# Performance work log

Hardware: AMD Instinct MI355X
Metric: run time of the kernel (lower is better)

Reference implementation:

```python
import jax, jax.numpy as jnp
import numpy as np

WIN = 11
SIGMA = 1.5
K1, K2 = 0.01, 0.03
DATA_RANGE = 1.0


def _gauss1d(size, sigma):
    coords = jnp.arange(size, dtype=jnp.float32) - size // 2
    g = jnp.exp(-(coords ** 2) / (2.0 * sigma ** 2))
    return g / g.sum()


def _blur(x, g):
    # Separable depthwise Gaussian blur, VALID padding, matching F.conv2d(groups=C).
    C = x.shape[1]
    w = g.astype(x.dtype)
    kh = jnp.broadcast_to(w.reshape(1, 1, WIN, 1), (C, 1, WIN, 1))  # blur along H
    kw = jnp.broadcast_to(w.reshape(1, 1, 1, WIN), (C, 1, 1, WIN))  # blur along W
    dn = ('NCHW', 'OIHW', 'NCHW')
    out = jax.lax.conv_general_dilated(x, kh, (1, 1), 'VALID',
                                       dimension_numbers=dn, feature_group_count=C)
    out = jax.lax.conv_general_dilated(out, kw, (1, 1), 'VALID',
                                       dimension_numbers=dn, feature_group_count=C)
    return out


def setup_inputs() -> dict:
    key = jax.random.key(0)
    k1, k2 = jax.random.split(key)
    shape = (16, 3, 512, 512)
    image1 = jax.random.uniform(k1, shape, dtype=jnp.float32)
    image2 = jax.random.uniform(k2, shape, dtype=jnp.float32)
    window = _gauss1d(WIN, SIGMA)
    return {"image1": image1, "image2": image2, "window": window}


def reference(image1, image2, window):
    c1 = (K1 * DATA_RANGE) ** 2
    c2 = (K2 * DATA_RANGE) ** 2
    mu1 = _blur(image1, window)
    mu2 = _blur(image2, window)
    mu1_sq = mu1 * mu1
    mu2_sq = mu2 * mu2
    mu1_mu2 = mu1 * mu2
    sigma1_sq = _blur(image1 * image1, window) - mu1_sq
    sigma2_sq = _blur(image2 * image2, window) - mu2_sq
    sigma12 = _blur(image1 * image2, window) - mu1_mu2
    cs_map = (2.0 * sigma12 + c2) / (sigma1_sq + sigma2_sq + c2)
    ssim_map = (2.0 * mu1_mu2 + c1) / (mu1_sq + mu2_sq + c1) * cs_map
    # flatten(2).mean(-1) then .mean() over (B,C) == full mean (uniform sizes)
    return ssim_map.mean()
```

## Files before the change

kernel.cpp:

```cpp
#include <hip/hip_runtime.h>

#define WIN   11
#define IW    512
#define IH    512
#define OW    502
#define OH    502
#define NCH   48
#define TW    54
#define SWC   64
#define SWP   66
#define CH    8
#define NCHUNK 8
#define SLABH (CH*NCHUNK)
#define NGX   10
#define NGY   8
#define PXL   7

typedef float v2f __attribute__((ext_vector_type(2)));

__device__ __forceinline__ float fast_rcp(float x) {
    return __builtin_amdgcn_rcpf(x);
}

template<bool EDGE>
__device__ __forceinline__ void ssim_slab(const float* __restrict__ p1,
                                          const float* __restrict__ p2,
                                          const float (&w)[WIN],
                                          v2f (*vbuf)[CH][SWP],
                                          int x0, int y0, int tid, float& acc)
{
    const int c = tid;
    int gx = x0 + c;
    if (EDGE) gx = min(gx, IW - 1);

    v2f h[10];
#pragma unroll
    for (int j = 0; j < 10; ++j) {
        int gy = y0 + j; if (EDGE) gy = min(gy, IH - 1);
        const int gidx = gy * IW + gx;
        h[j].x = p1[gidx];
        h[j].y = p2[gidx];
    }

    const int rh = tid >> 3;
    const int gg = tid & 7;
    const int xs = gg * PXL;
    const float c1 = 0.0001f;
    const float c2 = 0.0009f;

#pragma unroll
    for (int ci = 0; ci < NCHUNK; ++ci) {
        const int jbase = y0 + 10 + ci * CH;
        v2f n[CH];
#pragma unroll
        for (int j = 0; j < CH; ++j) {
            int gy = jbase + j; if (EDGE) gy = min(gy, IH - 1);
            const int gidx = gy * IW + gx;
            n[j].x = p1[gidx];
            n[j].y = p2[gidx];
        }

        v2f accA[CH], accB[CH];
#pragma unroll
        for (int r = 0; r < CH; ++r) {
            accA[r] = (v2f){0.f, 0.f};
            accB[r] = (v2f){0.f, 0.f};
        }
#pragma unroll
        for (int j = 0; j < CH + 10; ++j) {
            v2f ab = (j < 10) ? h[j] : n[j - 10];
            v2f st;
            st.x = fmaf(ab.x, ab.x, ab.y * ab.y);
            st.y = ab.x * ab.y;
#pragma unroll
            for (int k = 0; k < WIN; ++k) {
                const int r = j - k;
                if (r >= 0 && r < CH) {
                    v2f ws; ws.x = w[k]; ws.y = w[k];
                    accA[r] = __builtin_elementwise_fma(ws, ab, accA[r]);
                    accB[r] = __builtin_elementwise_fma(ws, st, accB[r]);
                }
            }
            if (j >= 10) {
                vbuf[0][j - 10][c] = accA[j - 10];
                vbuf[1][j - 10][c] = accB[j - 10];
            }
        }
#pragma unroll
        for (int j = 0; j < 10; ++j)
            h[j] = (j < 2) ? h[8 + j] : n[j - 2];

        __syncthreads();

        {
            v2f resA[PXL], resB[PXL];
#pragma unroll
            for (int q = 0; q < 2; ++q) {
                v2f x2[PXL + 10];
                const v2f* src = &vbuf[q][rh][xs];
#pragma unroll
                for (int t = 0; t < PXL + 10; ++t)
                    x2[t] = src[t];
#pragma unroll
                for (int o = 0; o < PXL; ++o) {
                    v2f s = {0.f, 0.f};
#pragma unroll
                    for (int k = 0; k < WIN; ++k) {
                        v2f ws; ws.x = w[k]; ws.y = w[k];
                        s = __builtin_elementwise_fma(ws, x2[o + k], s);
                    }
                    if (q == 0) resA[o] = s; else resB[o] = s;
                }
            }

            const int oy = y0 + ci * CH + rh;
#pragma unroll
            for (int o = 0; o < PXL; ++o) {
                const int tc = xs + o;
                bool valid = (tc < TW);
                if (EDGE) valid = valid && (oy < OH) && ((x0 + tc) < OW);
                if (valid) {
                    float m1 = resA[o].x, m2 = resA[o].y;
                    float mu11 = m1 * m1, mu22 = m2 * m2, mu12 = m1 * m2;
                    float sAB = resB[o].x - mu11 - mu22;
                    float s12 = resB[o].y - mu12;
                    float num = (2.f * mu12 + c1) * (2.f * s12 + c2);
                    float den = (mu11 + mu22 + c1) * (sAB + c2);
                    acc += num * fast_rcp(den);
                }
            }
        }
        __syncthreads();
    }
}

__global__ __launch_bounds__(64, 4)
void ssim_fused_kernel(const float* __restrict__ img1,
                       const float* __restrict__ img2,
                       const float* __restrict__ win,
                       float* __restrict__ partial)
{
    __shared__ __align__(16) v2f vbuf[2][CH][SWP];
    const int tid = threadIdx.x;
    const int ch = blockIdx.z;
    const int x0 = blockIdx.x * TW;
    const int y0 = blockIdx.y * SLABH;
    const float* __restrict__ p1 = img1 + (size_t)ch * (IW * IH);
    const float* __restrict__ p2 = img2 + (size_t)ch * (IW * IH);

    float w[WIN];
#pragma unroll
    for (int k = 0; k < WIN; ++k) w[k] = win[k];

    float acc = 0.f;
    const bool edge = (blockIdx.x == gridDim.x - 1) || (blockIdx.y == gridDim.y - 1);
    if (edge) ssim_slab<true >(p1, p2, w, vbuf, x0, y0, tid, acc);
    else      ssim_slab<false>(p1, p2, w, vbuf, x0, y0, tid, acc);

#pragma unroll
    for (int off = 32; off > 0; off >>= 1)
        acc += __shfl_down(acc, off, 64);
    if (tid == 0) {
        partial[(size_t)blockIdx.z * (gridDim.x * gridDim.y)
                + blockIdx.y * gridDim.x + blockIdx.x] = acc;
    }
}

__global__ __launch_bounds__(256)
void reduce_partials_kernel(const float* __restrict__ partial, int n4,
                            float* __restrict__ out, double inv_count)
{
    __shared__ double sd[256];
    const float4* p4 = reinterpret_cast<const float4*>(partial);
    double s = 0.0;
    for (int i = threadIdx.x; i < n4; i += 256) {
        float4 f = p4[i];
        s += (double)f.x + (double)f.y + (double)f.z + (double)f.w;
    }
    sd[threadIdx.x] = s;
    __syncthreads();
    for (int off = 128; off > 0; off >>= 1) {
        if (threadIdx.x < off) sd[threadIdx.x] += sd[threadIdx.x + off];
        __syncthreads();
    }
    if (threadIdx.x == 0)
        out[0] = (float)(sd[0] * inv_count);
}

extern "C" void kernel_launch(void* const* d_in, const int* in_sizes, int n_in,
                              void* d_out, int out_size, void* d_ws, size_t ws_size,
                              hipStream_t stream)
{
    const float* img1 = (const float*)d_in[0];
    const float* img2 = (const float*)d_in[1];
    const float* win  = (const float*)d_in[2];
    float* out = (float*)d_out;
    float* partial = (float*)d_ws;

    dim3 grid(NGX, NGY, NCH);
    dim3 block(64);

    ssim_fused_kernel<<<grid, block, 0, stream>>>(img1, img2, win, partial);

    const int nblocks = NGX * NGY * NCH;
    const double inv_count = 1.0 / ((double)NCH * OW * OH);
    reduce_partials_kernel<<<1, 256, 0, stream>>>(partial, nblocks / 4, out, inv_count);
}
```

Before: 47.55 us.

## Software-pipeline LDS reads for horizontal pass with next chunk's vertical pass

The SSIM slab loop is restructured so each chunk's horizontal-pass operands are issued as inline-asm ds_read_b64 loads. While those reads are in flight, the next chunk's global loads and vertical blur run and write into the same LDS buffer, followed by a single lgkmcnt wait. Both __syncthreads are dropped, which relies on the block being one 64-thread wavefront and on LDS operations executing in order. The aim is to hide LDS and global latency and remove barrier stalls. In exchange, the launch-bounds occupancy hint drops from 4 to 2 to allow the extra registers the held operands need.

```diff
diff --git a/kernel.cpp b/kernel.cpp
--- a/kernel.cpp
+++ b/kernel.cpp
@@ -22,6 +22,98 @@
     return __builtin_amdgcn_rcpf(x);
 }
 
+#define DSRD(dst, base, OFF) \
+    asm volatile("ds_read_b64 %0, %1 offset:" #OFF \
+                 : "=v"(dst) : "v"(base) : "memory")
+
+#define ISSUE17(x, b) \
+    DSRD(x[0],  b, 0);   DSRD(x[1],  b, 8);   DSRD(x[2],  b, 16);  \
+    DSRD(x[3],  b, 24);  DSRD(x[4],  b, 32);  DSRD(x[5],  b, 40);  \
+    DSRD(x[6],  b, 48);  DSRD(x[7],  b, 56);  DSRD(x[8],  b, 64);  \
+    DSRD(x[9],  b, 72);  DSRD(x[10], b, 80);  DSRD(x[11], b, 88);  \
+    DSRD(x[12], b, 96);  DSRD(x[13], b, 104); DSRD(x[14], b, 112); \
+    DSRD(x[15], b, 120); DSRD(x[16], b, 128);
+
+template<bool EDGE>
+__device__ __forceinline__ void load_rows(const float* __restrict__ p1,
+                                          const float* __restrict__ p2,
+                                          int gx, int jbase, v2f (&dst)[CH])
+{
+#pragma unroll
+    for (int j = 0; j < CH; ++j) {
+        int gy = jbase + j; if (EDGE) gy = min(gy, IH - 1);
+        const int gidx = gy * IW + gx;
+        dst[j].x = p1[gidx];
+        dst[j].y = p2[gidx];
+    }
+}
+
+__device__ __forceinline__ void vpass(const float (&w)[WIN],
+                                      v2f (&h)[10], const v2f (&n)[CH],
+                                      v2f (*vbuf)[CH][SWP], int c)
+{
+    v2f accA[CH], accB[CH];
+#pragma unroll
+    for (int r = 0; r < CH; ++r) {
+        accA[r] = (v2f){0.f, 0.f};
+        accB[r] = (v2f){0.f, 0.f};
+    }
+#pragma unroll
+    for (int j = 0; j < CH + 10; ++j) {
+        v2f ab = (j < 10) ? h[j] : n[j - 10];
+        v2f st;
+        st.x = fmaf(ab.x, ab.x, ab.y * ab.y);
+        st.y = ab.x * ab.y;
+#pragma unroll
+        for (int k = 0; k < WIN; ++k) {
+            const int r = j - k;
+            if (r >= 0 && r < CH) {
+                v2f ws; ws.x = w[k]; ws.y = w[k];
+                accA[r] = __builtin_elementwise_fma(ws, ab, accA[r]);
+                accB[r] = __builtin_elementwise_fma(ws, st, accB[r]);
+            }
+        }
+        if (j >= 10) {
+            vbuf[0][j - 10][c] = accA[j - 10];
+            vbuf[1][j - 10][c] = accB[j - 10];
+        }
+    }
+#pragma unroll
+    for (int j = 0; j < 10; ++j)
+        h[j] = (j < 2) ? h[8 + j] : n[j - 2];
+}
+
+template<bool EDGE>
+__device__ __forceinline__ void hcompute(const v2f (&xA)[17], const v2f (&xB)[17],
+                                         const float (&w)[WIN],
+                                         int oy, int x0, int xs, float& acc)
+{
+    const float c1 = 0.0001f;
+    const float c2 = 0.0009f;
+#pragma unroll
+    for (int o = 0; o < PXL; ++o) {
+        v2f sA = {0.f, 0.f}, sB = {0.f, 0.f};
+#pragma unroll
+        for (int k = 0; k < WIN; ++k) {
+            v2f ws; ws.x = w[k]; ws.y = w[k];
+            sA = __builtin_elementwise_fma(ws, xA[o + k], sA);
+            sB = __builtin_elementwise_fma(ws, xB[o + k], sB);
+        }
+        const int tc = xs + o;
+        bool valid = (tc < TW);
+        if (EDGE) valid = valid && (oy < OH) && ((x0 + tc) < OW);
+        if (valid) {
+            float m1 = sA.x, m2 = sA.y;
+            float mu11 = m1 * m1, mu22 = m2 * m2, mu12 = m1 * m2;
+            float sAB = sB.x - mu11 - mu22;
+            float s12 = sB.y - mu12;
+            float num = (2.f * mu12 + c1) * (2.f * s12 + c2);
+            float den = (mu11 + mu22 + c1) * (sAB + c2);
+            acc += num * fast_rcp(den);
+        }
+    }
+}
+
 template<bool EDGE>
 __device__ __forceinline__ void ssim_slab(const float* __restrict__ p1,
                                           const float* __restrict__ p2,
@@ -41,100 +133,37 @@
         h[j].x = p1[gidx];
         h[j].y = p2[gidx];
     }
+    v2f n[CH];
+    load_rows<EDGE>(p1, p2, gx, y0 + 10, n);
 
     const int rh = tid >> 3;
     const int gg = tid & 7;
     const int xs = gg * PXL;
-    const float c1 = 0.0001f;
-    const float c2 = 0.0009f;
+
+    const unsigned b0 = (unsigned)(uintptr_t)&vbuf[0][rh][xs];
+    const unsigned b1 = (unsigned)(uintptr_t)&vbuf[1][rh][xs];
+
+    vpass(w, h, n, vbuf, c);
 
 #pragma unroll
     for (int ci = 0; ci < NCHUNK; ++ci) {
-        const int jbase = y0 + 10 + ci * CH;
-        v2f n[CH];
-#pragma unroll
-        for (int j = 0; j < CH; ++j) {
-            int gy = jbase + j; if (EDGE) gy = min(gy, IH - 1);
-            const int gidx = gy * IW + gx;
-            n[j].x = p1[gidx];
-            n[j].y = p2[gidx];
-        }
-
-        v2f accA[CH], accB[CH];
-#pragma unroll
-        for (int r = 0; r < CH; ++r) {
-            accA[r] = (v2f){0.f, 0.f};
-            accB[r] = (v2f){0.f, 0.f};
-        }
-#pragma unroll
-        for (int j = 0; j < CH + 10; ++j) {
-            v2f ab = (j < 10) ? h[j] : n[j - 10];
-            v2f st;
-            st.x = fmaf(ab.x, ab.x, ab.y * ab.y);
-            st.y = ab.x * ab.y;
-#pragma unroll
-            for (int k = 0; k < WIN; ++k) {
-                const int r = j - k;
-                if (r >= 0 && r < CH) {
-                    v2f ws; ws.x = w[k]; ws.y = w[k];
-                    accA[r] = __builtin_elementwise_fma(ws, ab, accA[r]);
-                    accB[r] = __builtin_elementwise_fma(ws, st, accB[r]);
-                }
-            }
-            if (j >= 10) {
-                vbuf[0][j - 10][c] = accA[j - 10];
-                vbuf[1][j - 10][c] = accB[j - 10];
-            }
-        }
-#pragma unroll
-        for (int j = 0; j < 10; ++j)
-            h[j] = (j < 2) ? h[8 + j] : n[j - 2];
-
-        __syncthreads();
-
-        {
-            v2f resA[PXL], resB[PXL];
-#pragma unroll
-            for (int q = 0; q < 2; ++q) {
-                v2f x2[PXL + 10];
-                const v2f* src = &vbuf[q][rh][xs];
-#pragma unroll
-                for (int t = 0; t < PXL + 10; ++t)
-                    x2[t] = src[t];
-#pragma unroll
-                for (int o = 0; o < PXL; ++o) {
-                    v2f s = {0.f, 0.f};
-#pragma unroll
-                    for (int k = 0; k < WIN; ++k) {
-                        v2f ws; ws.x = w[k]; ws.y = w[k];
-                        s = __builtin_elementwise_fma(ws, x2[o + k], s);
-                    }
-                    if (q == 0) resA[o] = s; else resB[o] = s;
-                }
-            }
-
-            const int oy = y0 + ci * CH + rh;
-#pragma unroll
-            for (int o = 0; o < PXL; ++o) {
-                const int tc = xs + o;
-                bool valid = (tc < TW);
-                if (EDGE) valid = valid && (oy < OH) && ((x0 + tc) < OW);
-                if (valid) {
-                    float m1 = resA[o].x, m2 = resA[o].y;
-                    float mu11 = m1 * m1, mu22 = m2 * m2, mu12 = m1 * m2;
-                    float sAB = resB[o].x - mu11 - mu22;
-                    float s12 = resB[o].y - mu12;
-                    float num = (2.f * mu12 + c1) * (2.f * s12 + c2);
-                    float den = (mu11 + mu22 + c1) * (sAB + c2);
-                    acc += num * fast_rcp(den);
-                }
-            }
-        }
-        __syncthreads();
-    }
-}
-
-__global__ __launch_bounds__(64, 4)
+        v2f xA[17], xB[17];
+        ISSUE17(xA, b0);
+        ISSUE17(xB, b1);
+
+        if (ci + 1 < NCHUNK) {
+            load_rows<EDGE>(p1, p2, gx, y0 + 10 + (ci + 1) * CH, n);
+            vpass(w, h, n, vbuf, c);
+        }
+
+        asm volatile("s_waitcnt lgkmcnt(0)" ::: "memory");
+        __builtin_amdgcn_sched_barrier(0);
+
+        hcompute<EDGE>(xA, xB, w, y0 + ci * CH + rh, x0, xs, acc);
+    }
+}
+
+__global__ __launch_bounds__(64, 2)
 void ssim_fused_kernel(const float* __restrict__ img1,
                        const float* __restrict__ img2,
                        const float* __restrict__ win,
```

New measurement: 47.61 us. About the same (+0.1%).
